# Kernel tuning notes

Measured on AMD Instinct MI355X. Metric: run time of the kernel, lower is better.

Reference implementation:

```python
import jax, jax.numpy as jnp
import numpy as np
from jax import lax

B, T, D, H = 4096, 256, 18, 32


def setup_inputs() -> dict:
    key = jax.random.key(0)
    ks = jax.random.split(key, 9)
    s = 1.0 / np.sqrt(H)  # PyTorch LSTM init scale
    return {
        "batch": jax.random.normal(ks[0], (B, T, D), dtype=jnp.float32),
        "W_ih": jax.random.normal(ks[1], (4 * H, D), dtype=jnp.float32) * s,
        "W_hh": jax.random.normal(ks[2], (4 * H, H), dtype=jnp.float32) * s,
        "b_ih": jax.random.normal(ks[3], (4 * H,), dtype=jnp.float32) * s,
        "b_hh": jax.random.normal(ks[4], (4 * H,), dtype=jnp.float32) * s,
        "W1": jax.random.normal(ks[5], (512, H * T), dtype=jnp.float32) * 0.02,
        "b1": jax.random.normal(ks[6], (512,), dtype=jnp.float32) * 0.02,
        "W2": jax.random.normal(ks[7], (1, 512), dtype=jnp.float32) * 0.02,
        "b2": jax.random.normal(ks[8], (1,), dtype=jnp.float32) * 0.02,
    }


def _lstm(batch, W_ih, W_hh, b_ih, b_hh):
    b, t, _ = batch.shape
    h = batch.dtype.type
    # Precompute input projections for all timesteps: [B, T, 4H]
    x_proj = jnp.einsum('bti,gi->btg', batch, W_ih) + b_ih + b_hh
    W_hh_T = W_hh.T  # [H, 4H]

    def step(carry, xp):
        h_prev, c_prev = carry
        gates = xp + h_prev @ W_hh_T  # [B, 4H]
        i, f, g, o = jnp.split(gates, 4, axis=-1)  # PyTorch gate order i,f,g,o
        i = jax.nn.sigmoid(i)
        f = jax.nn.sigmoid(f)
        g = jnp.tanh(g)
        o = jax.nn.sigmoid(o)
        c = f * c_prev + i * g
        h_new = o * jnp.tanh(c)
        return (h_new, c), h_new

    h0 = jnp.zeros((b, H), dtype=batch.dtype)
    c0 = jnp.zeros((b, H), dtype=batch.dtype)
    _, hs = lax.scan(step, (h0, c0), x_proj.transpose(1, 0, 2))  # hs: [T, B, H]
    return hs.transpose(1, 0, 2)  # [B, T, H]


def reference(batch, W_ih, W_hh, b_ih, b_hh, W1, b1, W2, b2):
    hs = _lstm(batch, W_ih, W_hh, b_ih, b_hh)            # [B, T, H]
    flat = hs.reshape(hs.shape[0], -1)                   # [B, T*H]
    hid = jax.nn.relu(flat @ W1.T + b1)                  # [B, 512]
    return hid @ W2.T + b2                               # [B, 1]
```

## Files before the change

kernel.cpp:

```cpp
#include <hip/hip_runtime.h>
#include <hip/hip_bf16.h>
#include <stdint.h>

typedef float f32x4 __attribute__((ext_vector_type(4)));
typedef _Float16 half8 __attribute__((ext_vector_type(8)));

#define B_ 4096
#define T_ 256
#define D_ 18
#define H_ 32
#define GK 8192
#define GN 512
#define KSPLIT 4
#define SLOT 520

#define K1_ 1.442695041f
#define K2_ 2.885390082f
#define X2_ __builtin_amdgcn_exp2f
#define RCP_ __builtin_amdgcn_rcpf

__device__ __forceinline__ void ldsbar() {
  asm volatile("s_waitcnt lgkmcnt(0)\n\ts_barrier" ::: "memory");
}
__device__ __forceinline__ void fullbar() {
  asm volatile("s_waitcnt vmcnt(0) lgkmcnt(0)\n\ts_barrier" ::: "memory");
}
__device__ __forceinline__ void gl_lds16(const _Float16* g, _Float16* l) {
  __builtin_amdgcn_global_load_lds(
      (const __attribute__((address_space(1))) unsigned int*)g,
      (__attribute__((address_space(3))) unsigned int*)l, 16, 0, 0);
}

__global__ __launch_bounds__(256) void cvtw1_kernel(const float* __restrict__ w1,
                                                    unsigned short* __restrict__ dst) {
  int i = blockIdx.x * 256 + threadIdx.x;
  float4 v = ((const float4*)w1)[i];
  unsigned short a = __builtin_bit_cast(unsigned short, (_Float16)v.x);
  unsigned short b = __builtin_bit_cast(unsigned short, (_Float16)v.y);
  unsigned short c = __builtin_bit_cast(unsigned short, (_Float16)v.z);
  unsigned short d = __builtin_bit_cast(unsigned short, (_Float16)v.w);
  uint2 o; o.x = (unsigned)a | ((unsigned)b << 16); o.y = (unsigned)c | ((unsigned)d << 16);
  ((uint2*)dst)[i] = o;
}

__global__ __launch_bounds__(512) void lstm_kernel(
    const float* __restrict__ batch, const float* __restrict__ W_ih,
    const float* __restrict__ W_hh, const float* __restrict__ b_ih,
    const float* __restrict__ b_hh, _Float16* __restrict__ hs) {
  __shared__ _Float16 hist[16 * SLOT];
  __shared__ _Float16 xs[2 * 4096];

  const int tid = (int)threadIdx.x;
  const int lane = tid & 63;
  const int w = tid >> 6;
  const int lq = lane >> 4;
  const int lr = lane & 15;
  const int b0 = (int)blockIdx.x * 16;

  half8 wx, wh;
  {
    int grow = (lr & 3) * 32 + w * 4 + (lr >> 2);
#pragma unroll
    for (int j = 0; j < 8; ++j) {
      int k = lq * 8 + j;
      wx[j] = (k < D_) ? (_Float16)W_ih[grow * D_ + k] : (_Float16)0.0f;
      wh[j] = (_Float16)W_hh[grow * H_ + k];
    }
  }
  f32x4 bias4;
#pragma unroll
  for (int r = 0; r < 4; ++r) {
    int g = r * 32 + w * 4 + lq;
    bias4[r] = b_ih[g] + b_hh[g];
  }

  const int rdo = lr * 32 + ((lq ^ ((lr >> 1) & 3)) << 3);
  const int kcol = w * 4 + lq;
  const int wro = lr * 32 + ((((kcol >> 3) ^ ((lr >> 1) & 3))) << 3) + (kcol & 7);

  const int fe = tid >> 5;
  const int fs = (tid >> 2) & 7;
  const int fg = tid & 3;
  const int fl_rd = fs * SLOT + fe * 32 + ((fg ^ ((fe >> 1) & 3)) << 3);
  _Float16* fl_wp = hs + (size_t)(b0 + fe) * GK + fs * H_ + fg * 8;

  const int e0 = tid / 36, q0 = tid - e0 * 36;
  const int i1 = tid + 512;
  const int e1 = i1 / 36, q1 = i1 - e1 * 36;
  const float* xld0 = batch + (size_t)(b0 + e0) * (T_ * D_) + q0 * 4;
  const float* xld1 = batch + (size_t)(b0 + e1) * (T_ * D_) + q1 * 4;
  float4 xv0, xv1;

#define XLOAD(tb)                                                              \
  do {                                                                         \
    xv0 = *(const float4*)(xld0 + (tb) * 144);                                 \
    if (tid < 64) xv1 = *(const float4*)(xld1 + (tb) * 144);                   \
  } while (0)

#define XPUT(E, Q, V, buf)                                                     \
  do {                                                                         \
    int swz_ = ((E) >> 1) & 3;                                                 \
    _Pragma("unroll") for (int j = 0; j < 4; ++j) {                            \
      int f_ = (Q) * 4 + j;                                                    \
      int to_ = (f_ * 57) >> 10;                          \
      int d_ = f_ - to_ * 18;                                                  \
      float val_ = (j == 0) ? (V).x : (j == 1) ? (V).y : (j == 2) ? (V).z : (V).w; \
      xs[(buf) * 4096 + to_ * 512 + (E) * 32 + (((d_ >> 3) ^ swz_) << 3) + (d_ & 7)] = \
          (_Float16)val_;                                                      \
    }                                                                          \
  } while (0)

#define XSTORE(buf)                                                            \
  do {                                                                         \
    XPUT(e0, q0, xv0, buf);                                                    \
    if (tid < 64) XPUT(e1, q1, xv1, buf);                                      \
  } while (0)

#define STEP(tt, AXC, PRE)                                                     \
  do {                                                                         \
    _Float16* hrd = ((tt) == 0 ? po + 7 * SLOT : pr + ((tt)-1) * SLOT);        \
    half8 hf = *(const half8*)&hrd[rdo];                                       \
    f32x4 acc = __builtin_amdgcn_mfma_f32_16x16x32_f16(wh, hf, AXC, 0, 0, 0);  \
    PRE;                                                                       \
    float ei = X2_(-K1_ * acc[0]);                                             \
    float ef = X2_(-K1_ * acc[1]);                                             \
    float eg = X2_(-K2_ * acc[2]);                                             \
    float eo = X2_(-K1_ * acc[3]);                                             \
    float pi_ = (1.0f + ei) * (1.0f + eg);                                     \
    float num = fmaf(c, pi_, (1.0f + ef) * (1.0f - eg));                       \
    c = num * RCP_((1.0f + ef) * pi_);                                         \
    float ec = X2_(-K2_ * c);                                                  \
    float h = (1.0f - ec) * RCP_((1.0f + eo) * (1.0f + ec));                   \
    pr[(tt)*SLOT + wro] = (_Float16)h;                                         \
    ldsbar();                                                                  \
  } while (0)

  XLOAD(0);
  for (int i = tid; i < 16 * SLOT; i += 512) hist[i] = (_Float16)0.0f;
  for (int i = tid; i < 8192; i += 512) xs[i] = (_Float16)0.0f;
  ldsbar();
  XSTORE(0);
  XLOAD(1);
  ldsbar();

  float c = 0.0f;
  for (int blk = 0; blk < 32; ++blk) {
    const int p = blk & 1;
    _Float16* pr = hist + p * (8 * SLOT);
    _Float16* po = hist + (p ^ 1) * (8 * SLOT);
    const int xo = p * 4096;

    half8 xq[8];
#pragma unroll
    for (int j = 0; j < 8; ++j) xq[j] = *(const half8*)&xs[xo + j * 512 + rdo];
    f32x4 ax0, ax1;
    ax0 = __builtin_amdgcn_mfma_f32_16x16x32_f16(wx, xq[0], bias4, 0, 0, 0);

    STEP(0, ax0, ax1 = __builtin_amdgcn_mfma_f32_16x16x32_f16(wx, xq[1], bias4, 0, 0, 0));
    STEP(1, ax1, ax0 = __builtin_amdgcn_mfma_f32_16x16x32_f16(wx, xq[2], bias4, 0, 0, 0));
    STEP(2, ax0, ax1 = __builtin_amdgcn_mfma_f32_16x16x32_f16(wx, xq[3], bias4, 0, 0, 0));
    STEP(3, ax1, ax0 = __builtin_amdgcn_mfma_f32_16x16x32_f16(wx, xq[4], bias4, 0, 0, 0));
    if (blk < 31) XSTORE(p ^ 1);
    if (blk < 30) XLOAD(blk + 2);
    STEP(4, ax0, ax1 = __builtin_amdgcn_mfma_f32_16x16x32_f16(wx, xq[5], bias4, 0, 0, 0));
    if (blk) {
      half8 hv = *(const half8*)&hist[(p ^ 1) * (8 * SLOT) + fl_rd];
      *(half8*)(fl_wp + (size_t)(blk - 1) * (8 * H_)) = hv;
    }
    STEP(5, ax1, ax0 = __builtin_amdgcn_mfma_f32_16x16x32_f16(wx, xq[6], bias4, 0, 0, 0));
    STEP(6, ax0, ax1 = __builtin_amdgcn_mfma_f32_16x16x32_f16(wx, xq[7], bias4, 0, 0, 0));
    STEP(7, ax1, );
  }
  {
    half8 hv = *(const half8*)&hist[8 * SLOT + fl_rd];
    *(half8*)(fl_wp + (size_t)31 * (8 * H_)) = hv;
  }
#undef STEP
#undef XSTORE
#undef XPUT
#undef XLOAD
}

__global__ __launch_bounds__(256, 2) void gemm_kernel(
    const _Float16* __restrict__ Ahs, const _Float16* __restrict__ Bw1,
    float* __restrict__ part) {
  __shared__ _Float16 As[2 * 128 * 64];
  __shared__ _Float16 Bs[2 * 128 * 64];

  const int bid = (int)blockIdx.x;
  const int m0 = (bid & 31) << 7;
  const int n0 = ((bid >> 5) & 3) << 7;
  const int ksp = bid >> 7;
  const int k0 = ksp << 11;
  float* outp = part + (size_t)ksp * ((size_t)B_ * GN);

  const int tid = (int)threadIdx.x;
  const int lane = tid & 63, w = tid >> 6;
  const int wm = w & 1, wn = w >> 1;
  const int lq = lane >> 4, lr = lane & 15;

  const _Float16* gA[4]; const _Float16* gB[4];
  _Float16* lA[4]; _Float16* lB[4];
#pragma unroll
  for (int j = 0; j < 4; ++j) {
    int p = tid + 256 * j;
    int row = p >> 3, q = p & 7, cg = q ^ (row & 7);
    gA[j] = Ahs + (size_t)(m0 + row) * GK + k0 + cg * 8;
    gB[j] = Bw1 + (size_t)(n0 + row) * GK + k0 + cg * 8;
    int wbase = (w * 64 + 256 * j) * 8;
    lA[j] = As + wbase;
    lB[j] = Bs + wbase;
  }

  int offA[4][2], offB[4][2];
#pragma unroll
  for (int mt = 0; mt < 4; ++mt)
#pragma unroll
    for (int ks = 0; ks < 2; ++ks) {
      int m = wm * 64 + mt * 16 + lr;
      offA[mt][ks] = m * 64 + (((lq + ks * 4) ^ (m & 7)) << 3);
      int n = wn * 64 + mt * 16 + lr;
      offB[mt][ks] = n * 64 + (((lq + ks * 4) ^ (n & 7)) << 3);
    }

  f32x4 acc[4][4];
#pragma unroll
  for (int mt = 0; mt < 4; ++mt)
#pragma unroll
    for (int nt = 0; nt < 4; ++nt) {
      acc[mt][nt][0] = 0.f; acc[mt][nt][1] = 0.f;
      acc[mt][nt][2] = 0.f; acc[mt][nt][3] = 0.f;
    }

#define STAGE(POFF)                                                            \
  do {                                                                         \
    _Pragma("unroll") for (int j = 0; j < 4; ++j) {                            \
      gl_lds16(gA[j], lA[j] + (POFF));                                         \
      gl_lds16(gB[j], lB[j] + (POFF));                                         \
      gA[j] += 64; gB[j] += 64;                                                \
    }                                                                          \
  } while (0)

  STAGE(0);
  fullbar();

  for (int it = 0; it < 32; ++it) {
    const int POFF = (it & 1) * 8192;
    if (it < 31) STAGE(POFF ^ 8192);
    half8 af[4][2], bf[4][2];
#pragma unroll
    for (int mt = 0; mt < 4; ++mt)
#pragma unroll
      for (int ks = 0; ks < 2; ++ks) {
        af[mt][ks] = *(const half8*)&As[POFF + offA[mt][ks]];
        bf[mt][ks] = *(const half8*)&Bs[POFF + offB[mt][ks]];
      }
#pragma unroll
    for (int ks = 0; ks < 2; ++ks)
#pragma unroll
      for (int mt = 0; mt < 4; ++mt)
#pragma unroll
        for (int nt = 0; nt < 4; ++nt)
          acc[mt][nt] = __builtin_amdgcn_mfma_f32_16x16x32_f16(
              af[mt][ks], bf[nt][ks], acc[mt][nt], 0, 0, 0);
    fullbar();
  }
#undef STAGE

#pragma unroll
  for (int mt = 0; mt < 4; ++mt)
#pragma unroll
    for (int nt = 0; nt < 4; ++nt) {
      int n = n0 + wn * 64 + nt * 16 + lr;
#pragma unroll
      for (int r = 0; r < 4; ++r) {
        int m = m0 + wm * 64 + mt * 16 + lq * 4 + r;
        outp[(size_t)m * GN + n] = acc[mt][nt][r];
      }
    }
}

__global__ __launch_bounds__(256) void head_kernel(const float* __restrict__ part,
                                                   const float* __restrict__ b1,
                                                   const float* __restrict__ W2,
                                                   const float* __restrict__ b2,
                                                   float* __restrict__ out) {
  const int b = (int)(blockIdx.x * 4 + (threadIdx.x >> 6));
  const int l = (int)(threadIdx.x & 63);
  const size_t stride = (size_t)B_ * GN;
  const float4* b14 = (const float4*)b1;
  const float4* w4 = (const float4*)W2;
  float s = 0.0f;
#pragma unroll
  for (int p = 0; p < 2; ++p) {
    int i = p * 64 + l;
    float4 hv = ((const float4*)(part + (size_t)b * GN))[i];
#pragma unroll
    for (int sp = 1; sp < KSPLIT; ++sp) {
      float4 pv = ((const float4*)(part + sp * stride + (size_t)b * GN))[i];
      hv.x += pv.x; hv.y += pv.y; hv.z += pv.z; hv.w += pv.w;
    }
    float4 bv = b14[i], wv = w4[i];
    float t0 = fmaxf(hv.x + bv.x, 0.0f);
    float t1 = fmaxf(hv.y + bv.y, 0.0f);
    float t2 = fmaxf(hv.z + bv.z, 0.0f);
    float t3 = fmaxf(hv.w + bv.w, 0.0f);
    s = fmaf(t0, wv.x, s); s = fmaf(t1, wv.y, s);
    s = fmaf(t2, wv.z, s); s = fmaf(t3, wv.w, s);
  }
#pragma unroll
  for (int off = 32; off >= 1; off >>= 1) s += __shfl_xor(s, off);
  if (l == 0) out[b] = s + b2[0];
}

extern "C" void kernel_launch(void* const* d_in, const int* in_sizes, int n_in,
                              void* d_out, int out_size, void* d_ws, size_t ws_size,
                              hipStream_t stream) {
  const float* batch = (const float*)d_in[0];
  const float* W_ih = (const float*)d_in[1];
  const float* W_hh = (const float*)d_in[2];
  const float* b_ih = (const float*)d_in[3];
  const float* b_hh = (const float*)d_in[4];
  const float* W1 = (const float*)d_in[5];
  const float* b1 = (const float*)d_in[6];
  const float* W2 = (const float*)d_in[7];
  const float* b2 = (const float*)d_in[8];
  float* out = (float*)d_out;

  char* ws = (char*)d_ws;
  _Float16* hs = (_Float16*)ws;
  _Float16* w1h = (_Float16*)(ws + 67108864);
  float* part = (float*)(ws + 67108864 + 8388608);

  cvtw1_kernel<<<4096, 256, 0, stream>>>(W1, (unsigned short*)w1h);
  lstm_kernel<<<256, 512, 0, stream>>>(batch, W_ih, W_hh, b_ih, b_hh, hs);
  gemm_kernel<<<512, 256, 0, stream>>>(hs, w1h, part);
  head_kernel<<<1024, 256, 0, stream>>>(part, b1, W2, b2, out);
}
```

Before: 228.0 us.

## Fuse W1 GEMM and head into LSTM kernel, dropping hs round-trip

The LSTM kernel now multiplies each 8-timestep block of hidden states with the fp16 W1 slice directly from LDS using MFMA, accumulating the 512-wide hidden layer per block, then applies bias, ReLU, the W2 dot product and a cross-wave reduction to write the output. This removes the 64MB hs write and reread, the separate split-K GEMM, the partial-sum buffer and the head kernel. In exchange each of the 256 blocks streams the full 8MB W1 from global/L2 inside the latency-critical recurrence, which adds register pressure and memory traffic alongside the serial LSTM steps.

Result: slower. 383.6 us (+68.2%).

```diff
diff --git a/kernel.cpp b/kernel.cpp
--- a/kernel.cpp
+++ b/kernel.cpp
@@ -11,7 +11,6 @@
 #define H_ 32
 #define GK 8192
 #define GN 512
-#define KSPLIT 4
 #define SLOT 520
 
 #define K1_ 1.442695041f
@@ -21,14 +20,6 @@
 
 __device__ __forceinline__ void ldsbar() {
   asm volatile("s_waitcnt lgkmcnt(0)\n\ts_barrier" ::: "memory");
-}
-__device__ __forceinline__ void fullbar() {
-  asm volatile("s_waitcnt vmcnt(0) lgkmcnt(0)\n\ts_barrier" ::: "memory");
-}
-__device__ __forceinline__ void gl_lds16(const _Float16* g, _Float16* l) {
-  __builtin_amdgcn_global_load_lds(
-      (const __attribute__((address_space(1))) unsigned int*)g,
-      (__attribute__((address_space(3))) unsigned int*)l, 16, 0, 0);
 }
 
 __global__ __launch_bounds__(256) void cvtw1_kernel(const float* __restrict__ w1,
@@ -46,7 +37,9 @@
 __global__ __launch_bounds__(512) void lstm_kernel(
     const float* __restrict__ batch, const float* __restrict__ W_ih,
     const float* __restrict__ W_hh, const float* __restrict__ b_ih,
-    const float* __restrict__ b_hh, _Float16* __restrict__ hs) {
+    const float* __restrict__ b_hh, const _Float16* __restrict__ w1h,
+    const float* __restrict__ b1, const float* __restrict__ W2,
+    const float* __restrict__ b2, float* __restrict__ out) {
   __shared__ _Float16 hist[16 * SLOT];
   __shared__ _Float16 xs[2 * 4096];
 
@@ -78,11 +71,16 @@
   const int kcol = w * 4 + lq;
   const int wro = lr * 32 + ((((kcol >> 3) ^ ((lr >> 1) & 3))) << 3) + (kcol & 7);
 
-  const int fe = tid >> 5;
-  const int fs = (tid >> 2) & 7;
-  const int fg = tid & 3;
-  const int fl_rd = fs * SLOT + fe * 32 + ((fg ^ ((fe >> 1) & 3)) << 3);
-  _Float16* fl_wp = hs + (size_t)(b0 + fe) * GK + fs * H_ + fg * 8;
+  const _Float16* wp[4];
+#pragma unroll
+  for (int nt = 0; nt < 4; ++nt)
+    wp[nt] = w1h + (size_t)(w * 64 + nt * 16 + lr) * GK + lq * 8;
+
+  f32x4 gacc[4];
+#pragma unroll
+  for (int nt = 0; nt < 4; ++nt) {
+    gacc[nt][0] = 0.f; gacc[nt][1] = 0.f; gacc[nt][2] = 0.f; gacc[nt][3] = 0.f;
+  }
 
   const int e0 = tid / 36, q0 = tid - e0 * 36;
   const int i1 = tid + 512;
@@ -116,12 +114,24 @@
     if (tid < 64) XPUT(e1, q1, xv1, buf);                                      \
   } while (0)
 
-#define STEP(tt, AXC, PRE)                                                     \
+#define STEP(tt, AXC, WFC, WFN, PRE)                                           \
   do {                                                                         \
     _Float16* hrd = ((tt) == 0 ? po + 7 * SLOT : pr + ((tt)-1) * SLOT);        \
     half8 hf = *(const half8*)&hrd[rdo];                                       \
     f32x4 acc = __builtin_amdgcn_mfma_f32_16x16x32_f16(wh, hf, AXC, 0, 0, 0);  \
     PRE;                                                                       \
+    if (blk) {                                                                 \
+      if ((tt) < 7) {                                                          \
+        _Pragma("unroll") for (int nt = 0; nt < 4; ++nt) {                     \
+          WFN[nt] = *(const half8*)wp[nt];                                     \
+          wp[nt] += 32;                                                        \
+        }                                                                      \
+      }                                                                        \
+      half8 gb = *(const half8*)&po[(tt) * SLOT + rdo];                        \
+      _Pragma("unroll") for (int nt = 0; nt < 4; ++nt)                         \
+        gacc[nt] = __builtin_amdgcn_mfma_f32_16x16x32_f16(WFC[nt], gb,         \
+                                                          gacc[nt], 0, 0, 0); \
+    }                                                                          \
     float ei = X2_(-K1_ * acc[0]);                                             \
     float ef = X2_(-K1_ * acc[1]);                                             \
     float eg = X2_(-K2_ * acc[2]);                                             \
@@ -156,161 +166,68 @@
     f32x4 ax0, ax1;
     ax0 = __builtin_amdgcn_mfma_f32_16x16x32_f16(wx, xq[0], bias4, 0, 0, 0);
 
-    STEP(0, ax0, ax1 = __builtin_amdgcn_mfma_f32_16x16x32_f16(wx, xq[1], bias4, 0, 0, 0));
-    STEP(1, ax1, ax0 = __builtin_amdgcn_mfma_f32_16x16x32_f16(wx, xq[2], bias4, 0, 0, 0));
-    STEP(2, ax0, ax1 = __builtin_amdgcn_mfma_f32_16x16x32_f16(wx, xq[3], bias4, 0, 0, 0));
-    STEP(3, ax1, ax0 = __builtin_amdgcn_mfma_f32_16x16x32_f16(wx, xq[4], bias4, 0, 0, 0));
+    half8 wfA[4], wfB[4];
+    if (blk) {
+#pragma unroll
+      for (int nt = 0; nt < 4; ++nt) {
+        wfA[nt] = *(const half8*)wp[nt];
+        wp[nt] += 32;
+      }
+    }
+
+    STEP(0, ax0, wfA, wfB, ax1 = __builtin_amdgcn_mfma_f32_16x16x32_f16(wx, xq[1], bias4, 0, 0, 0));
+    STEP(1, ax1, wfB, wfA, ax0 = __builtin_amdgcn_mfma_f32_16x16x32_f16(wx, xq[2], bias4, 0, 0, 0));
+    STEP(2, ax0, wfA, wfB, ax1 = __builtin_amdgcn_mfma_f32_16x16x32_f16(wx, xq[3], bias4, 0, 0, 0));
+    STEP(3, ax1, wfB, wfA, ax0 = __builtin_amdgcn_mfma_f32_16x16x32_f16(wx, xq[4], bias4, 0, 0, 0));
     if (blk < 31) XSTORE(p ^ 1);
     if (blk < 30) XLOAD(blk + 2);
-    STEP(4, ax0, ax1 = __builtin_amdgcn_mfma_f32_16x16x32_f16(wx, xq[5], bias4, 0, 0, 0));
-    if (blk) {
-      half8 hv = *(const half8*)&hist[(p ^ 1) * (8 * SLOT) + fl_rd];
-      *(half8*)(fl_wp + (size_t)(blk - 1) * (8 * H_)) = hv;
-    }
-    STEP(5, ax1, ax0 = __builtin_amdgcn_mfma_f32_16x16x32_f16(wx, xq[6], bias4, 0, 0, 0));
-    STEP(6, ax0, ax1 = __builtin_amdgcn_mfma_f32_16x16x32_f16(wx, xq[7], bias4, 0, 0, 0));
-    STEP(7, ax1, );
-  }
+    STEP(4, ax0, wfA, wfB, ax1 = __builtin_amdgcn_mfma_f32_16x16x32_f16(wx, xq[5], bias4, 0, 0, 0));
+    STEP(5, ax1, wfB, wfA, ax0 = __builtin_amdgcn_mfma_f32_16x16x32_f16(wx, xq[6], bias4, 0, 0, 0));
+    STEP(6, ax0, wfA, wfB, ax1 = __builtin_amdgcn_mfma_f32_16x16x32_f16(wx, xq[7], bias4, 0, 0, 0));
+    STEP(7, ax1, wfB, wfA, );
+  }
+
   {
-    half8 hv = *(const half8*)&hist[8 * SLOT + fl_rd];
-    *(half8*)(fl_wp + (size_t)31 * (8 * H_)) = hv;
+    const _Float16* pe = hist + 8 * SLOT;
+#pragma unroll
+    for (int tt = 0; tt < 8; ++tt) {
+      half8 gb = *(const half8*)&pe[tt * SLOT + rdo];
+#pragma unroll
+      for (int nt = 0; nt < 4; ++nt) {
+        half8 ga = *(const half8*)wp[nt];
+        wp[nt] += 32;
+        gacc[nt] = __builtin_amdgcn_mfma_f32_16x16x32_f16(ga, gb, gacc[nt], 0, 0, 0);
+      }
+    }
+  }
+
+  float s = 0.0f;
+#pragma unroll
+  for (int nt = 0; nt < 4; ++nt) {
+    float4 b1v = ((const float4*)b1)[w * 16 + nt * 4 + lq];
+    float4 w2v = ((const float4*)W2)[w * 16 + nt * 4 + lq];
+#pragma unroll
+    for (int r = 0; r < 4; ++r) {
+      float t = gacc[nt][r] + ((const float*)&b1v)[r];
+      t = fmaxf(t, 0.0f);
+      s = fmaf(t, ((const float*)&w2v)[r], s);
+    }
+  }
+  s += __shfl_xor(s, 16);
+  s += __shfl_xor(s, 32);
+  float* red = (float*)xs;
+  if (lane < 16) red[w * 16 + lane] = s;
+  ldsbar();
+  if (tid < 16) {
+    float t = 0.0f;
+#pragma unroll
+    for (int ww = 0; ww < 8; ++ww) t += red[ww * 16 + tid];
+    out[b0 + tid] = t + b2[0];
   }
 #undef STEP
 #undef XSTORE
 #undef XPUT
 #undef XLOAD
-}
-
-__global__ __launch_bounds__(256, 2) void gemm_kernel(
-    const _Float16* __restrict__ Ahs, const _Float16* __restrict__ Bw1,
-    float* __restrict__ part) {
-  __shared__ _Float16 As[2 * 128 * 64];
-  __shared__ _Float16 Bs[2 * 128 * 64];
-
-  const int bid = (int)blockIdx.x;
-  const int m0 = (bid & 31) << 7;
-  const int n0 = ((bid >> 5) & 3) << 7;
-  const int ksp = bid >> 7;
-  const int k0 = ksp << 11;
-  float* outp = part + (size_t)ksp * ((size_t)B_ * GN);
-
-  const int tid = (int)threadIdx.x;
-  const int lane = tid & 63, w = tid >> 6;
-  const int wm = w & 1, wn = w >> 1;
-  const int lq = lane >> 4, lr = lane & 15;
-
-  const _Float16* gA[4]; const _Float16* gB[4];
-  _Float16* lA[4]; _Float16* lB[4];
-#pragma unroll
-  for (int j = 0; j < 4; ++j) {
-    int p = tid + 256 * j;
-    int row = p >> 3, q = p & 7, cg = q ^ (row & 7);
-    gA[j] = Ahs + (size_t)(m0 + row) * GK + k0 + cg * 8;
-    gB[j] = Bw1 + (size_t)(n0 + row) * GK + k0 + cg * 8;
-    int wbase = (w * 64 + 256 * j) * 8;
-    lA[j] = As + wbase;
-    lB[j] = Bs + wbase;
-  }
-
-  int offA[4][2], offB[4][2];
-#pragma unroll
-  for (int mt = 0; mt < 4; ++mt)
-#pragma unroll
-    for (int ks = 0; ks < 2; ++ks) {
-      int m = wm * 64 + mt * 16 + lr;
-      offA[mt][ks] = m * 64 + (((lq + ks * 4) ^ (m & 7)) << 3);
-      int n = wn * 64 + mt * 16 + lr;
-      offB[mt][ks] = n * 64 + (((lq + ks * 4) ^ (n & 7)) << 3);
-    }
-
-  f32x4 acc[4][4];
-#pragma unroll
-  for (int mt = 0; mt < 4; ++mt)
-#pragma unroll
-    for (int nt = 0; nt < 4; ++nt) {
-      acc[mt][nt][0] = 0.f; acc[mt][nt][1] = 0.f;
-      acc[mt][nt][2] = 0.f; acc[mt][nt][3] = 0.f;
-    }
-
-#define STAGE(POFF)                                                            \
-  do {                                                                         \
-    _Pragma("unroll") for (int j = 0; j < 4; ++j) {                            \
-      gl_lds16(gA[j], lA[j] + (POFF));                                         \
-      gl_lds16(gB[j], lB[j] + (POFF));                                         \
-      gA[j] += 64; gB[j] += 64;                                                \
-    }                                                                          \
-  } while (0)
-
-  STAGE(0);
-  fullbar();
-
-  for (int it = 0; it < 32; ++it) {
-    const int POFF = (it & 1) * 8192;
-    if (it < 31) STAGE(POFF ^ 8192);
-    half8 af[4][2], bf[4][2];
-#pragma unroll
-    for (int mt = 0; mt < 4; ++mt)
-#pragma unroll
-      for (int ks = 0; ks < 2; ++ks) {
-        af[mt][ks] = *(const half8*)&As[POFF + offA[mt][ks]];
-        bf[mt][ks] = *(const half8*)&Bs[POFF + offB[mt][ks]];
-      }
-#pragma unroll
-    for (int ks = 0; ks < 2; ++ks)
-#pragma unroll
-      for (int mt = 0; mt < 4; ++mt)
-#pragma unroll
-        for (int nt = 0; nt < 4; ++nt)
-          acc[mt][nt] = __builtin_amdgcn_mfma_f32_16x16x32_f16(
-              af[mt][ks], bf[nt][ks], acc[mt][nt], 0, 0, 0);
-    fullbar();
-  }
-#undef STAGE
-
-#pragma unroll
-  for (int mt = 0; mt < 4; ++mt)
-#pragma unroll
-    for (int nt = 0; nt < 4; ++nt) {
-      int n = n0 + wn * 64 + nt * 16 + lr;
-#pragma unroll
-      for (int r = 0; r < 4; ++r) {
-        int m = m0 + wm * 64 + mt * 16 + lq * 4 + r;
-        outp[(size_t)m * GN + n] = acc[mt][nt][r];
-      }
-    }
-}
-
-__global__ __launch_bounds__(256) void head_kernel(const float* __restrict__ part,
-                                                   const float* __restrict__ b1,
-                                                   const float* __restrict__ W2,
-                                                   const float* __restrict__ b2,
-                                                   float* __restrict__ out) {
-  const int b = (int)(blockIdx.x * 4 + (threadIdx.x >> 6));
-  const int l = (int)(threadIdx.x & 63);
-  const size_t stride = (size_t)B_ * GN;
-  const float4* b14 = (const float4*)b1;
-  const float4* w4 = (const float4*)W2;
-  float s = 0.0f;
-#pragma unroll
-  for (int p = 0; p < 2; ++p) {
-    int i = p * 64 + l;
-    float4 hv = ((const float4*)(part + (size_t)b * GN))[i];
-#pragma unroll
-    for (int sp = 1; sp < KSPLIT; ++sp) {
-      float4 pv = ((const float4*)(part + sp * stride + (size_t)b * GN))[i];
-      hv.x += pv.x; hv.y += pv.y; hv.z += pv.z; hv.w += pv.w;
-    }
-    float4 bv = b14[i], wv = w4[i];
-    float t0 = fmaxf(hv.x + bv.x, 0.0f);
-    float t1 = fmaxf(hv.y + bv.y, 0.0f);
-    float t2 = fmaxf(hv.z + bv.z, 0.0f);
-    float t3 = fmaxf(hv.w + bv.w, 0.0f);
-    s = fmaf(t0, wv.x, s); s = fmaf(t1, wv.y, s);
-    s = fmaf(t2, wv.z, s); s = fmaf(t3, wv.w, s);
-  }
-#pragma unroll
-  for (int off = 32; off >= 1; off >>= 1) s += __shfl_xor(s, off);
-  if (l == 0) out[b] = s + b2[0];
 }
 
 extern "C" void kernel_launch(void* const* d_in, const int* in_sizes, int n_in,
@@ -328,12 +245,9 @@
   float* out = (float*)d_out;
 
   char* ws = (char*)d_ws;
-  _Float16* hs = (_Float16*)ws;
-  _Float16* w1h = (_Float16*)(ws + 67108864);
-  float* part = (float*)(ws + 67108864 + 8388608);
+  _Float16* w1h = (_Float16*)ws;
 
   cvtw1_kernel<<<4096, 256, 0, stream>>>(W1, (unsigned short*)w1h);
-  lstm_kernel<<<256, 512, 0, stream>>>(batch, W_ih, W_hh, b_ih, b_hh, hs);
-  gemm_kernel<<<512, 256, 0, stream>>>(hs, w1h, part);
-  head_kernel<<<1024, 256, 0, stream>>>(part, b1, W2, b2, out);
-}
+  lstm_kernel<<<256, 512, 0, stream>>>(batch, W_ih, W_hh, b_ih, b_hh,
+                                       w1h, b1, W2, b2, out);
+}
```
